# Performance work log

Hardware: AMD Instinct MI355X
Metric: run time of the kernel (lower is better)

## Reference

```python
import jax, jax.numpy as jnp
import numpy as np

NUM_HEADS = 32
HEAD_DIM = 64
ROPE_THETA = 10000.0


def _rope_cos_sin(position_ids, head_dim, theta):
    # inv_freq: [head_dim/2]
    half = head_dim // 2
    inv_freq = 1.0 / (theta ** (jnp.arange(0, half, dtype=jnp.float32) * 2.0 / head_dim))
    angles = position_ids.astype(jnp.float32)[..., None] * inv_freq  # [B,S,half]
    return jnp.cos(angles), jnp.sin(angles)


def _apply_rope(x, cos, sin):
    # x: [B,S,H,hd]; cos/sin: [B,S,half] -> broadcast over heads (rotate-half, Llama style)
    half = x.shape[-1] // 2
    x1, x2 = x[..., :half], x[..., half:]
    c = cos[:, :, None, :]
    s = sin[:, :, None, :]
    return jnp.concatenate([x1 * c - x2 * s, x2 * c + x1 * s], axis=-1)


def setup_inputs() -> dict:
    key = jax.random.key(0)
    ks = jax.random.split(key, 8)
    B, S, D = 2, 2048, 2048
    hidden_states = jax.random.normal(ks[0], (B, S, D), dtype=jnp.float32)
    # causal additive mask (is_causal=False in IpexSDP; mask carries causality)
    causal = jnp.tril(jnp.ones((S, S), dtype=jnp.bool_))
    attention_mask = jnp.where(causal, 0.0, -1e9).astype(jnp.float32)[None, None, :, :]
    attention_mask = jnp.broadcast_to(attention_mask, (B, 1, S, S))
    position_ids = jnp.broadcast_to(jnp.arange(S, dtype=jnp.int64)[None, :], (B, S))
    scale = 0.02
    qkv_w = jax.random.normal(ks[1], (3, D, D), dtype=jnp.float32) * scale
    qkv_b = jax.random.normal(ks[2], (3, D), dtype=jnp.float32) * scale
    o_w = jax.random.normal(ks[3], (D, D), dtype=jnp.float32) * scale
    o_b = jax.random.normal(ks[4], (D,), dtype=jnp.float32) * scale
    residual = jax.random.normal(ks[5], (B, S, D), dtype=jnp.float32)
    return {
        'hidden_states': hidden_states,
        'attention_mask': attention_mask,
        'position_ids': position_ids,
        'qkv_w': qkv_w,
        'qkv_b': qkv_b,
        'o_w': o_w,
        'o_b': o_b,
        'residual': residual,
    }


def reference(hidden_states, attention_mask, position_ids, qkv_w, qkv_b, o_w, o_b, residual):
    B, S, D = hidden_states.shape
    H, hd = NUM_HEADS, HEAD_DIM
    # fused QKV projection (weights stored transposed: x @ W), matching mm_qkv_out
    qkv = jnp.einsum('bsd,tde->tbse', hidden_states, qkv_w) + qkv_b[:, None, None, :]
    q = qkv[0].reshape(B, S, H, hd)
    k = qkv[1].reshape(B, S, H, hd)
    v = qkv[2].reshape(B, S, H, hd)
    cos, sin = _rope_cos_sin(position_ids, hd, ROPE_THETA)
    q = _apply_rope(q, cos, sin)
    k = _apply_rope(k, cos, sin)
    scale = 1.0 / jnp.sqrt(jnp.asarray(hd, dtype=hidden_states.dtype))
    # [B,H,S,S]
    scores = jnp.einsum('bqhd,bkhd->bhqk', q, k) * scale + attention_mask
    probs = jax.nn.softmax(scores, axis=-1)
    attn = jnp.einsum('bhqk,bkhd->bqhd', probs, v).reshape(B, S, D)
    # o-proj fused with bias + residual add (matmul_add_add)
    out = attn @ o_w + o_b + residual
    return out
```

## Files before the change

### kernel.cpp

```cpp
#include <hip/hip_runtime.h>
#include <stdint.h>
#include <stdio.h>

#define D_MODEL 2048
#define SEQ     2048
#define NHEADS  32
#define HDIM    64
#define BATCH   2
#define BH      (BATCH * NHEADS)
#define GK      2048

typedef unsigned short u16;
typedef unsigned int   u32;
typedef __attribute__((ext_vector_type(8))) short short8;
typedef __attribute__((ext_vector_type(4))) short s16x4;
typedef __attribute__((ext_vector_type(4))) float f32x4;
typedef __attribute__((ext_vector_type(4))) u32   u32x4;
typedef __attribute__((ext_vector_type(2))) u32   u32x2;

__device__ __forceinline__ float bf2f(u16 x) {
  union { u32 u; float f; } c; c.u = ((u32)x) << 16; return c.f;
}
__device__ __forceinline__ u16 f2bf(float f) {
  union { float f; u32 u; } c; c.f = f;
  u32 u = c.u;
  return (u16)((u + 0x7FFFu + ((u >> 16) & 1u)) >> 16);
}
__device__ __forceinline__ u32 fbits(float f) {
  union { float f; u32 u; } c; c.f = f; return c.u;
}

typedef const __attribute__((address_space(1))) u32* gas_t;
typedef __attribute__((address_space(3))) u32* las_t;
__device__ __forceinline__ void gll16(const void* g, void* l) {
  __builtin_amdgcn_global_load_lds((gas_t)g, (las_t)l, 16, 0, 0);
}
__device__ __forceinline__ u32 lds_addr(const void* p) {
  return (u32)(size_t)(const __attribute__((address_space(3))) void*)p;
}
__device__ __forceinline__ short8 ds_read128(u32 addr) {
  short8 r;
  asm volatile("ds_read_b128 %0, %1" : "=v"(r) : "v"(addr));
  return r;
}

__device__ __forceinline__ void swiz_mn(int pid, int nx, int& mtile, int& ntile) {
  int chunk = 8 * nx;
  int grp = pid / chunk, loc = pid - grp * chunk;
  mtile = grp * 8 + (loc & 7);
  ntile = loc >> 3;
}

__global__ __launch_bounds__(256) void cvt_k(const float* __restrict__ in,
                                             u16* __restrict__ out) {
  int id = blockIdx.x * 256 + threadIdx.x;
  f32x4 v = *(const f32x4*)&in[(size_t)id * 4];
  alignas(8) u16 o[4];
#pragma unroll
  for (int j = 0; j < 4; j++) o[j] = f2bf(v[j]);
  *(u32x2*)&out[(size_t)id * 4] = *(const u32x2*)o;
}

__global__ __launch_bounds__(256) void transpose_cvt_k(const float* __restrict__ qkv_w,
                                                       const float* __restrict__ o_w,
                                                       u16* __restrict__ outT) {
  __shared__ u16 tile[64][72];
  const int z = blockIdx.z;
  const float* inz = (z < 3) ? qkv_w + (size_t)z * D_MODEL * D_MODEL : o_w;
  u16* outz = outT + (size_t)z * D_MODEL * D_MODEL;
  const int r0 = blockIdx.y * 64, c0 = blockIdx.x * 64;
  const int t = threadIdx.x;
  const int lrow = t >> 4, lcol4 = (t & 15) * 4;
#pragma unroll
  for (int i = 0; i < 4; i++) {
    int r = lrow + i * 16;
    f32x4 v = *(const f32x4*)&inz[(size_t)(r0 + r) * D_MODEL + (c0 + lcol4)];
#pragma unroll
    for (int j = 0; j < 4; j++) tile[r][lcol4 + j] = f2bf(v[j]);
  }
  __syncthreads();
  const int row = t >> 3, col8 = (t & 7) * 8;
#pragma unroll
  for (int i = 0; i < 2; i++) {
    int r = row + i * 32;
    alignas(16) u16 vals[8];
#pragma unroll
    for (int j = 0; j < 8; j++) vals[j] = tile[col8 + j][r];
    *(u32x4*)&outz[(size_t)(c0 + r) * D_MODEL + (r0 + col8)] = *(const u32x4*)vals;
  }
}

__device__ __forceinline__ void gemm128(const u16* __restrict__ A, const u16* __restrict__ BT,
                                        int m0, int n0, u16* As, u16* Bs, f32x4 acc[4][4]) {
  const int t = threadIdx.x;
  const int lane = t & 63, w = t >> 6;
  const int quad = lane >> 4, l16 = lane & 15;
  const int wr = w >> 1, wc = w & 1;
  const int ldr = lane >> 2, ldc = (lane & 3) * 8;
#pragma unroll
  for (int mt = 0; mt < 4; mt++)
#pragma unroll
    for (int nt = 0; nt < 4; nt++)
#pragma unroll
      for (int i = 0; i < 4; i++) acc[mt][nt][i] = 0.0f;

  for (int k0 = 0; k0 < GK; k0 += 32) {
    __syncthreads();
#pragma unroll
    for (int i = 0; i < 2; i++) {
      int rbase = w * 32 + i * 16;
      gll16(&A[(size_t)(m0 + rbase + ldr) * GK + k0 + ldc], &As[rbase * 32]);
      gll16(&BT[(size_t)(n0 + rbase + ldr) * GK + k0 + ldc], &Bs[rbase * 32]);
    }
    __syncthreads();
    short8 af[4], bf[4];
#pragma unroll
    for (int mt = 0; mt < 4; mt++)
      af[mt] = *(const short8*)&As[(wr * 64 + mt * 16 + l16) * 32 + quad * 8];
#pragma unroll
    for (int nt = 0; nt < 4; nt++)
      bf[nt] = *(const short8*)&Bs[(wc * 64 + nt * 16 + l16) * 32 + quad * 8];
#pragma unroll
    for (int mt = 0; mt < 4; mt++)
#pragma unroll
      for (int nt = 0; nt < 4; nt++)
        acc[mt][nt] = __builtin_amdgcn_mfma_f32_16x16x32_bf16(af[mt], bf[nt], acc[mt][nt], 0, 0, 0);
  }
}


__device__ __forceinline__ void stage_half(const u16* __restrict__ src, int rowbase, int k0,
                                           u16* tile, int h, int w, int srl, int scol) {
  u16* ldsb = tile + h * (128 * 64);
  const u16* g0 = &src[(size_t)(rowbase + h * 128 + srl) * GK + k0 + scol];
  const u16* g1 = &src[(size_t)(rowbase + h * 128 + srl + 8) * GK + k0 + scol];
  gll16(g0, (char*)ldsb + w * 2048);
  gll16(g1, (char*)ldsb + w * 2048 + 1024);
}

#define LGKM0_FENCE  do { asm volatile("s_waitcnt lgkmcnt(0)"); __builtin_amdgcn_sched_barrier(0); } while (0)

__global__ __launch_bounds__(512, 1) void qkv_gemm256_k(const u16* __restrict__ A,
                                                        const u16* __restrict__ BT,
                                                        const float* __restrict__ bias,
                                                        u16* __restrict__ Qb, u16* __restrict__ Kb,
                                                        u16* __restrict__ Vbt) {
  __shared__ u16 As[2][256 * 64];
  __shared__ u16 Bs[2][256 * 64];
  const int t = threadIdx.x, w = t >> 6, lane = t & 63;
  const int quad = lane >> 4, l16 = lane & 15;
  const int wr = w >> 2, wc = w & 3;
  int mtile, ntile;
  swiz_mn(blockIdx.x, 24, mtile, ntile);
  const int m0 = mtile * 256, n0 = ntile * 256;
  const int srl = w * 16 + (lane >> 3);
  const int scol = (((lane & 7) ^ (lane >> 3)) << 3);

  const u32 asb0 = lds_addr(As[0]), asb1 = lds_addr(As[1]);
  const u32 bsb0 = lds_addr(Bs[0]), bsb1 = lds_addr(Bs[1]);
  const u32 xorc = (u32)((l16 & 7) << 4);
  const u32 cq0 = (u32)(quad * 16) ^ xorc;
  const u32 cq1 = (u32)(64 + quad * 16) ^ xorc;

  f32x4 acc[8][4];
#pragma unroll
  for (int mf = 0; mf < 8; mf++)
#pragma unroll
    for (int nf = 0; nf < 4; nf++)
#pragma unroll
      for (int i = 0; i < 4; i++) acc[mf][nf][i] = 0.0f;

  const int NT = GK / 64;
  stage_half(A, m0, 0, As[0], 0, w, srl, scol);
  stage_half(A, m0, 0, As[0], 1, w, srl, scol);
  stage_half(BT, n0, 0, Bs[0], 0, w, srl, scol);
  stage_half(BT, n0, 0, Bs[0], 1, w, srl, scol);
  stage_half(A, m0, 64, As[1], 0, w, srl, scol);
  stage_half(A, m0, 64, As[1], 1, w, srl, scol);
  asm volatile("s_waitcnt vmcnt(4)");
  __builtin_amdgcn_sched_barrier(0);
  __builtin_amdgcn_s_barrier();

  for (int kt = 0; kt < NT; kt++) {
    const int cur = kt & 1;
    const u32 aA = cur ? asb1 : asb0;
    const u32 aB = cur ? bsb1 : bsb0;
    u16* Acur = cur ? (u16*)As[1] : (u16*)As[0];
    u16* Bnxt = cur ? (u16*)Bs[0] : (u16*)Bs[1];
    short8 af[8][2], bf[4][2];
#pragma unroll
    for (int mf = 0; mf < 4; mf++) {
      u32 rb = aA + (u32)((wr * 128 + mf * 16 + l16) * 128);
      af[mf][0] = ds_read128(rb + cq0);
      af[mf][1] = ds_read128(rb + cq1);
    }
#pragma unroll
    for (int nf = 0; nf < 2; nf++) {
      u32 rb = aB + (u32)((wc * 64 + nf * 16 + l16) * 128);
      bf[nf][0] = ds_read128(rb + cq0);
      bf[nf][1] = ds_read128(rb + cq1);
    }
    if (kt + 1 < NT) stage_half(BT, n0, (kt + 1) * 64, Bnxt, 0, w, srl, scol);
    __builtin_amdgcn_s_barrier();
    LGKM0_FENCE;
    __builtin_amdgcn_s_setprio(1);
#pragma unroll
    for (int mf = 0; mf < 4; mf++)
#pragma unroll
      for (int nf = 0; nf < 2; nf++) {
        acc[mf][nf] = __builtin_amdgcn_mfma_f32_16x16x32_bf16(af[mf][0], bf[nf][0], acc[mf][nf], 0, 0, 0);
        acc[mf][nf] = __builtin_amdgcn_mfma_f32_16x16x32_bf16(af[mf][1], bf[nf][1], acc[mf][nf], 0, 0, 0);
      }
    __builtin_amdgcn_s_setprio(0);
    __builtin_amdgcn_s_barrier();
    __builtin_amdgcn_sched_barrier(0);
#pragma unroll
    for (int mf = 4; mf < 8; mf++) {
      u32 rb = aA + (u32)((wr * 128 + mf * 16 + l16) * 128);
      af[mf][0] = ds_read128(rb + cq0);
      af[mf][1] = ds_read128(rb + cq1);
    }
    if (kt + 1 < NT) stage_half(BT, n0, (kt + 1) * 64, Bnxt, 1, w, srl, scol);
    __builtin_amdgcn_s_barrier();
    LGKM0_FENCE;
    __builtin_amdgcn_s_setprio(1);
#pragma unroll
    for (int mf = 4; mf < 8; mf++)
#pragma unroll
      for (int nf = 0; nf < 2; nf++) {
        acc[mf][nf] = __builtin_amdgcn_mfma_f32_16x16x32_bf16(af[mf][0], bf[nf][0], acc[mf][nf], 0, 0, 0);
        acc[mf][nf] = __builtin_amdgcn_mfma_f32_16x16x32_bf16(af[mf][1], bf[nf][1], acc[mf][nf], 0, 0, 0);
      }
    __builtin_amdgcn_s_setprio(0);
    __builtin_amdgcn_s_barrier();
    __builtin_amdgcn_sched_barrier(0);
#pragma unroll
    for (int nf = 2; nf < 4; nf++) {
      u32 rb = aB + (u32)((wc * 64 + nf * 16 + l16) * 128);
      bf[nf][0] = ds_read128(rb + cq0);
      bf[nf][1] = ds_read128(rb + cq1);
    }
    if (kt + 2 < NT) stage_half(A, m0, (kt + 2) * 64, Acur, 0, w, srl, scol);
    __builtin_amdgcn_s_barrier();
    LGKM0_FENCE;
    __builtin_amdgcn_s_setprio(1);
#pragma unroll
    for (int mf = 0; mf < 4; mf++)
#pragma unroll
      for (int nf = 2; nf < 4; nf++) {
        acc[mf][nf] = __builtin_amdgcn_mfma_f32_16x16x32_bf16(af[mf][0], bf[nf][0], acc[mf][nf], 0, 0, 0);
        acc[mf][nf] = __builtin_amdgcn_mfma_f32_16x16x32_bf16(af[mf][1], bf[nf][1], acc[mf][nf], 0, 0, 0);
      }
    __builtin_amdgcn_s_setprio(0);
    __builtin_amdgcn_s_barrier();
    __builtin_amdgcn_sched_barrier(0);
    if (kt + 2 < NT) stage_half(A, m0, (kt + 2) * 64, Acur, 1, w, srl, scol);
    __builtin_amdgcn_s_barrier();
    __builtin_amdgcn_s_setprio(1);
#pragma unroll
    for (int mf = 4; mf < 8; mf++)
#pragma unroll
      for (int nf = 2; nf < 4; nf++) {
        acc[mf][nf] = __builtin_amdgcn_mfma_f32_16x16x32_bf16(af[mf][0], bf[nf][0], acc[mf][nf], 0, 0, 0);
        acc[mf][nf] = __builtin_amdgcn_mfma_f32_16x16x32_bf16(af[mf][1], bf[nf][1], acc[mf][nf], 0, 0, 0);
      }
    __builtin_amdgcn_s_setprio(0);
    if (kt + 2 < NT) {
      asm volatile("s_waitcnt vmcnt(4)");
    } else {
      asm volatile("s_waitcnt vmcnt(0)");
    }
    __builtin_amdgcn_sched_barrier(0);
    __builtin_amdgcn_s_barrier();
    __builtin_amdgcn_sched_barrier(0);
  }

  const int tsel = n0 >> 11;
  if (tsel < 2) {
    u16* dst = tsel ? Kb : Qb;
#pragma unroll
    for (int p = 0; p < 2; p++) {
      int nlo = n0 + wc * 64 + p * 16 + l16;
      float blo = bias[nlo], bhi = bias[nlo + 32];
      int j = p * 16 + l16;
      float inv = __expf((float)j * -0.28782313662425572f);
      int h = (nlo & 2047) >> 6;
#pragma unroll
      for (int mf = 0; mf < 8; mf++) {
#pragma unroll
        for (int r = 0; r < 4; r++) {
          int m = m0 + wr * 128 + mf * 16 + quad * 4 + r;
          int b = m >> 11, s = m & (SEQ - 1);
          float sn, cs;
          __sincosf((float)s * inv, &sn, &cs);
          float x1 = acc[mf][p][r] + blo;
          float x2 = acc[mf][p + 2][r] + bhi;
          size_t base = ((size_t)((b * NHEADS + h) * SEQ + s)) * HDIM;
          dst[base + j]      = f2bf(x1 * cs - x2 * sn);
          dst[base + j + 32] = f2bf(x2 * cs + x1 * sn);
        }
      }
    }
  } else {
#pragma unroll
    for (int nf = 0; nf < 4; nf++) {
      int n = n0 + wc * 64 + nf * 16 + l16;
      float bv = bias[n];
      int e = n & 2047, h = e >> 6, d = e & 63;
#pragma unroll
      for (int mf = 0; mf < 8; mf++) {
        int m0r = m0 + wr * 128 + mf * 16 + quad * 4;
        int b = m0r >> 11, s0 = m0r & (SEQ - 1);
        alignas(8) u16 o4[4];
#pragma unroll
        for (int r = 0; r < 4; r++) o4[r] = f2bf(acc[mf][nf][r] + bv);
        *(u32x2*)&Vbt[((size_t)((b * NHEADS + h) * HDIM + d)) * SEQ + s0] = *(const u32x2*)o4;
      }
    }
  }
}

__global__ __launch_bounds__(256) void oproj_gemm_k(const u16* __restrict__ A, const u16* __restrict__ BT,
                                                    const float* __restrict__ bias,
                                                    const float* __restrict__ resid,
                                                    float* __restrict__ out) {
  __shared__ u16 As[128 * 32], Bs[128 * 32];
  f32x4 acc[4][4];
  int mtile, ntile;
  swiz_mn(blockIdx.x, 16, mtile, ntile);
  const int m0 = mtile * 128, n0 = ntile * 128;
  gemm128(A, BT, m0, n0, As, Bs, acc);
  const int t = threadIdx.x, lane = t & 63, quad = lane >> 4, l16 = lane & 15;
  const int w = t >> 6, wr = w >> 1, wc = w & 1;
#pragma unroll
  for (int nt = 0; nt < 4; nt++) {
    int n = n0 + wc * 64 + nt * 16 + l16;
    float bv = bias[n];
#pragma unroll
    for (int mt = 0; mt < 4; mt++) {
#pragma unroll
      for (int r = 0; r < 4; r++) {
        int m = m0 + wr * 64 + mt * 16 + quad * 4 + r;
        size_t oi = (size_t)m * D_MODEL + n;
        out[oi] = acc[mt][nt][r] + bv + resid[oi];
      }
    }
  }
}

__global__ __launch_bounds__(256, 2) void attn_k(const u16* __restrict__ Qb,
                                                 const u16* __restrict__ Kb,
                                                 const u16* __restrict__ Vbt,
                                                 u16* __restrict__ attn) {
  __shared__ u16 smem[128 * 72];
  u16* Ks = smem;
  u16* Vt = smem + 64 * 72;
  const int blk = blockIdx.x;
  const int bh = blk & 63, pi = blk >> 6;
  const int b = bh >> 5, h = bh & 31;
  const int t = threadIdx.x, w = t >> 6, lane = t & 63, quad = lane >> 4, l16 = lane & 15;
  const int qbT[2] = { pi * 128, (15 - pi) * 128 };
  const int qwT[2] = { qbT[0] + w * 32, qbT[1] + w * 32 };
  const size_t bho = (size_t)bh * SEQ * HDIM;
  const size_t vbo = (size_t)bh * HDIM * SEQ;
  const int kend = qbT[1] + 128;

  short8 qf[2][2][2];
#pragma unroll
  for (int Ti = 0; Ti < 2; Ti++)
#pragma unroll
    for (int qt = 0; qt < 2; qt++)
#pragma unroll
      for (int kd = 0; kd < 2; kd++) {
        short8 v = *(const short8*)&Qb[bho + (size_t)(qwT[Ti] + qt * 16 + l16) * HDIM + kd * 32 + quad * 8];
#pragma unroll
        for (int i = 0; i < 8; i++) {
          float f = bf2f((u16)v[i]) * 0.125f;
          v[i] = (short)f2bf(f);
        }
        qf[Ti][qt][kd] = v;
      }

  f32x4 Oacc[2][4][2];
  float mrow[2][2] = {{-1e30f, -1e30f}, {-1e30f, -1e30f}};
  float lrow[2][2] = {{0.0f, 0.0f}, {0.0f, 0.0f}};
#pragma unroll
  for (int Ti = 0; Ti < 2; Ti++)
#pragma unroll
    for (int dt = 0; dt < 4; dt++)
#pragma unroll
      for (int qt = 0; qt < 2; qt++)
#pragma unroll
        for (int i = 0; i < 4; i++) Oacc[Ti][dt][qt][i] = 0.0f;

  const int srow = t >> 3, sc8 = (t & 7) * 8;
  u32x4 kreg[2], vreg[2];

#pragma unroll
  for (int j = 0; j < 2; j++) {
    kreg[j] = *(const u32x4*)&Kb[bho + (size_t)(srow + j * 32) * HDIM + sc8];
    vreg[j] = *(const u32x4*)&Vbt[vbo + (size_t)(srow + j * 32) * SEQ + sc8];
  }
#pragma unroll
  for (int j = 0; j < 2; j++) {
    *(u32x4*)&Ks[(srow + j * 32) * 72 + sc8] = kreg[j];
    *(u32x4*)&Vt[(srow + j * 32) * 72 + sc8] = vreg[j];
  }
  __syncthreads();

  for (int key0 = 0; key0 < kend; key0 += 64) {
    const int nxt = key0 + 64;
    if (nxt < kend) {
#pragma unroll
      for (int j = 0; j < 2; j++) {
        kreg[j] = *(const u32x4*)&Kb[bho + (size_t)(nxt + srow + j * 32) * HDIM + sc8];
        vreg[j] = *(const u32x4*)&Vbt[vbo + (size_t)(srow + j * 32) * SEQ + nxt + sc8];
      }
    }
#pragma unroll
    for (int Ti = 0; Ti < 2; Ti++) {
      const int qw = qwT[Ti];
      if (key0 <= qw + 31) {
        const int lim = qw + 31 - key0;
        int nkt = (lim >> 4) + 1; if (nkt > 4) nkt = 4;
        f32x4 sacc[4][2];
#pragma unroll
        for (int kt = 0; kt < 4; kt++) {
          if (kt < nkt) {
            short8 kf0 = *(const short8*)&Ks[(kt * 16 + l16) * 72 + quad * 8];
            short8 kf1 = *(const short8*)&Ks[(kt * 16 + l16) * 72 + 32 + quad * 8];
#pragma unroll
            for (int qt = 0; qt < 2; qt++) {
              f32x4 z = {0.0f, 0.0f, 0.0f, 0.0f};
              z = __builtin_amdgcn_mfma_f32_16x16x32_bf16(kf0, qf[Ti][qt][0], z, 0, 0, 0);
              z = __builtin_amdgcn_mfma_f32_16x16x32_bf16(kf1, qf[Ti][qt][1], z, 0, 0, 0);
              sacc[kt][qt] = z;
            }
          }
        }
        if (key0 + 63 > qw) {
#pragma unroll
          for (int qt = 0; qt < 2; qt++) {
            int qrow = qw + qt * 16 + l16;
#pragma unroll
            for (int kt = 0; kt < 4; kt++)
              if (kt < nkt)
#pragma unroll
                for (int r = 0; r < 4; r++)
                  if (key0 + kt * 16 + quad * 4 + r > qrow) sacc[kt][qt][r] = -1e30f;
          }
        }
        float alpha[2];
#pragma unroll
        for (int qt = 0; qt < 2; qt++) {
          float mx = -1e30f;
#pragma unroll
          for (int kt = 0; kt < 4; kt++)
            if (kt < nkt)
#pragma unroll
              for (int r = 0; r < 4; r++) mx = fmaxf(mx, sacc[kt][qt][r]);
          mx = fmaxf(mx, __shfl_xor(mx, 16));
          mx = fmaxf(mx, __shfl_xor(mx, 32));
          float mnew = fmaxf(mrow[Ti][qt], mx);
          alpha[qt] = __expf(mrow[Ti][qt] - mnew);
          mrow[Ti][qt] = mnew;
          float rsum = 0.0f;
#pragma unroll
          for (int kt = 0; kt < 4; kt++)
            if (kt < nkt)
#pragma unroll
              for (int r = 0; r < 4; r++) {
                float pv = __expf(sacc[kt][qt][r] - mnew);
                sacc[kt][qt][r] = pv;
                rsum += pv;
              }
          rsum += __shfl_xor(rsum, 16);
          rsum += __shfl_xor(rsum, 32);
          lrow[Ti][qt] = lrow[Ti][qt] * alpha[qt] + rsum;
        }
#pragma unroll
        for (int dt = 0; dt < 4; dt++)
#pragma unroll
          for (int qt = 0; qt < 2; qt++)
#pragma unroll
            for (int r = 0; r < 4; r++) Oacc[Ti][dt][qt][r] *= alpha[qt];
#pragma unroll
        for (int kt = 0; kt < 4; kt++) {
          if (kt < nkt) {
            s16x4 pk[2];
#pragma unroll
            for (int qt = 0; qt < 2; qt++) {
              u32 a0 = fbits(sacc[kt][qt][0]) + 0x8000u;
              u32 a1 = fbits(sacc[kt][qt][1]) + 0x8000u;
              u32 a2 = fbits(sacc[kt][qt][2]) + 0x8000u;
              u32 a3 = fbits(sacc[kt][qt][3]) + 0x8000u;
              union { u32 u[2]; s16x4 s; } pc;
              pc.u[0] = __builtin_amdgcn_perm(a1, a0, 0x07060302u);
              pc.u[1] = __builtin_amdgcn_perm(a3, a2, 0x07060302u);
              pk[qt] = pc.s;
            }
            s16x4 vf[4];
#pragma unroll
            for (int dt = 0; dt < 4; dt++)
              vf[dt] = *(const s16x4*)&Vt[(dt * 16 + l16) * 72 + kt * 16 + quad * 4];
#pragma unroll
            for (int dt = 0; dt < 4; dt++)
#pragma unroll
              for (int qt = 0; qt < 2; qt++)
                Oacc[Ti][dt][qt] = __builtin_amdgcn_mfma_f32_16x16x16bf16_1k(vf[dt], pk[qt], Oacc[Ti][dt][qt], 0, 0, 0);
          }
        }
      }
    }
    __syncthreads();
    if (nxt < kend) {
#pragma unroll
      for (int j = 0; j < 2; j++) {
        *(u32x4*)&Ks[(srow + j * 32) * 72 + sc8] = kreg[j];
        *(u32x4*)&Vt[(srow + j * 32) * 72 + sc8] = vreg[j];
      }
      __syncthreads();
    }
  }

#pragma unroll
  for (int Ti = 0; Ti < 2; Ti++) {
    float invl[2] = {1.0f / lrow[Ti][0], 1.0f / lrow[Ti][1]};
#pragma unroll
    for (int dt = 0; dt < 4; dt++)
#pragma unroll
      for (int qt = 0; qt < 2; qt++)
#pragma unroll
        for (int r = 0; r < 4; r++)
          smem[(w * 32 + qt * 16 + l16) * 72 + dt * 16 + quad * 4 + r] =
              f2bf(Oacc[Ti][dt][qt][r] * invl[qt]);
    __syncthreads();
#pragma unroll
    for (int ii = 0; ii < 4; ii++) {
      int chunk = t + ii * 256;
      int row = chunk >> 3, g = chunk & 7;
      *(u32x4*)&attn[((size_t)(b * SEQ + qbT[Ti] + row)) * D_MODEL + h * 64 + g * 8] =
          *(const u32x4*)&smem[row * 72 + g * 8];
    }
    __syncthreads();
  }
}

extern "C" void kernel_launch(void* const* d_in, const int* in_sizes, int n_in,
                              void* d_out, int out_size, void* d_ws, size_t ws_size,
                              hipStream_t stream) {
  (void)in_sizes; (void)n_in; (void)out_size;
  const float* hidden = (const float*)d_in[0];
  const float* qkv_w = (const float*)d_in[3];
  const float* qkv_b = (const float*)d_in[4];
  const float* o_w   = (const float*)d_in[5];
  const float* o_b   = (const float*)d_in[6];
  const float* resid = (const float*)d_in[7];
  float* out = (float*)d_out;

  u16* ws = (u16*)d_ws;
  size_t off = 0;
  u16* hidb  = ws + off; off += (size_t)BATCH * SEQ * D_MODEL;
  u16* qkvT  = ws + off; off += (size_t)3 * D_MODEL * D_MODEL;
  u16* owT   = ws + off; off += (size_t)D_MODEL * D_MODEL;
  u16* Qb    = ws + off; off += (size_t)BH * SEQ * HDIM;
  u16* Kb    = ws + off; off += (size_t)BH * SEQ * HDIM;
  u16* Vbt   = ws + off; off += (size_t)BH * SEQ * HDIM;
  u16* attnb = ws + off; off += (size_t)BATCH * SEQ * D_MODEL;
  if (ws_size < off * sizeof(u16)) {
    fprintf(stderr, "kernel_launch: workspace too small: need %zu bytes, have %zu\n",
            off * sizeof(u16), ws_size);
    return;
  }
  (void)owT;

  cvt_k<<<(BATCH * SEQ * D_MODEL) / (4 * 256), 256, 0, stream>>>(hidden, hidb);
  transpose_cvt_k<<<dim3(32, 32, 4), 256, 0, stream>>>(qkv_w, o_w, qkvT);
  qkv_gemm256_k<<<16 * 24, 512, 0, stream>>>(hidb, qkvT, qkv_b, Qb, Kb, Vbt);
  attn_k<<<BH * 8, 256, 0, stream>>>(Qb, Kb, Vbt, attnb);
  oproj_gemm_k<<<16 * 32, 256, 0, stream>>>(attnb, owT, o_b, resid, out);
}
```

Baseline: 426.1 us.

## Restructure QKV GEMM K-loop: issue all LDS reads upfront with immediate offsets, fewer barriers

The QKV GEMM main loop now issues all A and B fragment LDS reads for a k-step at the start, using ds_read_b128 with immediate offsets from precomputed base addresses. It then waits on partial lgkmcnt counts so MFMA groups can start while later reads are still in flight. The B-tile global-to-LDS stages are merged into one point and the A-tile stages into another, which drops several workgroup barriers per iteration. This cuts address arithmetic and synchronisation stalls. The cost is more live fragment registers and a hand-counted lgkmcnt sequence that must stay consistent with the interleaved global_load_lds traffic.

```diff
diff --git a/kernel.cpp b/kernel.cpp
--- a/kernel.cpp
+++ b/kernel.cpp
@@ -38,9 +38,10 @@
 __device__ __forceinline__ u32 lds_addr(const void* p) {
   return (u32)(size_t)(const __attribute__((address_space(3))) void*)p;
 }
-__device__ __forceinline__ short8 ds_read128(u32 addr) {
+template <int OFF>
+__device__ __forceinline__ short8 ds_read128o(u32 addr) {
   short8 r;
-  asm volatile("ds_read_b128 %0, %1" : "=v"(r) : "v"(addr));
+  asm volatile("ds_read_b128 %0, %1 offset:%2" : "=v"(r) : "v"(addr), "i"(OFF));
   return r;
 }
 
@@ -138,7 +139,7 @@
   gll16(g1, (char*)ldsb + w * 2048 + 1024);
 }
 
-#define LGKM0_FENCE  do { asm volatile("s_waitcnt lgkmcnt(0)"); __builtin_amdgcn_sched_barrier(0); } while (0)
+#define SBAR0 __builtin_amdgcn_sched_barrier(0)
 
 __global__ __launch_bounds__(512, 1) void qkv_gemm256_k(const u16* __restrict__ A,
                                                         const u16* __restrict__ BT,
@@ -161,6 +162,8 @@
   const u32 xorc = (u32)((l16 & 7) << 4);
   const u32 cq0 = (u32)(quad * 16) ^ xorc;
   const u32 cq1 = (u32)(64 + quad * 16) ^ xorc;
+  const u32 rowA = (u32)((wr * 128 + l16) * 128);
+  const u32 rowB = (u32)((wc * 64 + l16) * 128);
 
   f32x4 acc[8][4];
 #pragma unroll
@@ -178,31 +181,33 @@
   stage_half(A, m0, 64, As[1], 0, w, srl, scol);
   stage_half(A, m0, 64, As[1], 1, w, srl, scol);
   asm volatile("s_waitcnt vmcnt(4)");
-  __builtin_amdgcn_sched_barrier(0);
+  SBAR0;
   __builtin_amdgcn_s_barrier();
+
+#define RD_A(mf, kh) af[mf][kh] = ds_read128o<(mf) * 2048>((kh) ? bA1 : bA0)
+#define RD_B(nf, kh) bf[nf][kh] = ds_read128o<(nf) * 2048>((kh) ? bB1 : bB0)
 
   for (int kt = 0; kt < NT; kt++) {
     const int cur = kt & 1;
-    const u32 aA = cur ? asb1 : asb0;
-    const u32 aB = cur ? bsb1 : bsb0;
+    const u32 aAb = cur ? asb1 : asb0;
+    const u32 aBb = cur ? bsb1 : bsb0;
+    const u32 bA0 = aAb + rowA + cq0, bA1 = aAb + rowA + cq1;
+    const u32 bB0 = aBb + rowB + cq0, bB1 = aBb + rowB + cq1;
     u16* Acur = cur ? (u16*)As[1] : (u16*)As[0];
     u16* Bnxt = cur ? (u16*)Bs[0] : (u16*)Bs[1];
     short8 af[8][2], bf[4][2];
-#pragma unroll
-    for (int mf = 0; mf < 4; mf++) {
-      u32 rb = aA + (u32)((wr * 128 + mf * 16 + l16) * 128);
-      af[mf][0] = ds_read128(rb + cq0);
-      af[mf][1] = ds_read128(rb + cq1);
-    }
-#pragma unroll
-    for (int nf = 0; nf < 2; nf++) {
-      u32 rb = aB + (u32)((wc * 64 + nf * 16 + l16) * 128);
-      bf[nf][0] = ds_read128(rb + cq0);
-      bf[nf][1] = ds_read128(rb + cq1);
-    }
-    if (kt + 1 < NT) stage_half(BT, n0, (kt + 1) * 64, Bnxt, 0, w, srl, scol);
-    __builtin_amdgcn_s_barrier();
-    LGKM0_FENCE;
+    RD_A(0, 0); RD_A(0, 1); RD_A(1, 0); RD_A(1, 1);
+    RD_A(2, 0); RD_A(2, 1); RD_A(3, 0); RD_A(3, 1);
+    RD_B(0, 0); RD_B(0, 1); RD_B(1, 0); RD_B(1, 1);
+    RD_A(4, 0); RD_A(4, 1); RD_A(5, 0); RD_A(5, 1);
+    RD_A(6, 0); RD_A(6, 1); RD_A(7, 0); RD_A(7, 1);
+    RD_B(2, 0); RD_B(2, 1); RD_B(3, 0); RD_B(3, 1);
+    if (kt + 1 < NT) {
+      stage_half(BT, n0, (kt + 1) * 64, Bnxt, 0, w, srl, scol);
+      stage_half(BT, n0, (kt + 1) * 64, Bnxt, 1, w, srl, scol);
+    }
+    asm volatile("s_waitcnt lgkmcnt(12)");
+    SBAR0;
     __builtin_amdgcn_s_setprio(1);
 #pragma unroll
     for (int mf = 0; mf < 4; mf++)
@@ -212,17 +217,8 @@
         acc[mf][nf] = __builtin_amdgcn_mfma_f32_16x16x32_bf16(af[mf][1], bf[nf][1], acc[mf][nf], 0, 0, 0);
       }
     __builtin_amdgcn_s_setprio(0);
-    __builtin_amdgcn_s_barrier();
-    __builtin_amdgcn_sched_barrier(0);
-#pragma unroll
-    for (int mf = 4; mf < 8; mf++) {
-      u32 rb = aA + (u32)((wr * 128 + mf * 16 + l16) * 128);
-      af[mf][0] = ds_read128(rb + cq0);
-      af[mf][1] = ds_read128(rb + cq1);
-    }
-    if (kt + 1 < NT) stage_half(BT, n0, (kt + 1) * 64, Bnxt, 1, w, srl, scol);
-    __builtin_amdgcn_s_barrier();
-    LGKM0_FENCE;
+    asm volatile("s_waitcnt lgkmcnt(4)");
+    SBAR0;
     __builtin_amdgcn_s_setprio(1);
 #pragma unroll
     for (int mf = 4; mf < 8; mf++)
@@ -233,32 +229,16 @@
       }
     __builtin_amdgcn_s_setprio(0);
     __builtin_amdgcn_s_barrier();
-    __builtin_amdgcn_sched_barrier(0);
-#pragma unroll
-    for (int nf = 2; nf < 4; nf++) {
-      u32 rb = aB + (u32)((wc * 64 + nf * 16 + l16) * 128);
-      bf[nf][0] = ds_read128(rb + cq0);
-      bf[nf][1] = ds_read128(rb + cq1);
-    }
-    if (kt + 2 < NT) stage_half(A, m0, (kt + 2) * 64, Acur, 0, w, srl, scol);
-    __builtin_amdgcn_s_barrier();
-    LGKM0_FENCE;
+    SBAR0;
+    if (kt + 2 < NT) {
+      stage_half(A, m0, (kt + 2) * 64, Acur, 0, w, srl, scol);
+      stage_half(A, m0, (kt + 2) * 64, Acur, 1, w, srl, scol);
+    }
+    asm volatile("s_waitcnt lgkmcnt(0)");
+    SBAR0;
     __builtin_amdgcn_s_setprio(1);
 #pragma unroll
-    for (int mf = 0; mf < 4; mf++)
-#pragma unroll
-      for (int nf = 2; nf < 4; nf++) {
-        acc[mf][nf] = __builtin_amdgcn_mfma_f32_16x16x32_bf16(af[mf][0], bf[nf][0], acc[mf][nf], 0, 0, 0);
-        acc[mf][nf] = __builtin_amdgcn_mfma_f32_16x16x32_bf16(af[mf][1], bf[nf][1], acc[mf][nf], 0, 0, 0);
-      }
-    __builtin_amdgcn_s_setprio(0);
-    __builtin_amdgcn_s_barrier();
-    __builtin_amdgcn_sched_barrier(0);
-    if (kt + 2 < NT) stage_half(A, m0, (kt + 2) * 64, Acur, 1, w, srl, scol);
-    __builtin_amdgcn_s_barrier();
-    __builtin_amdgcn_s_setprio(1);
-#pragma unroll
-    for (int mf = 4; mf < 8; mf++)
+    for (int mf = 0; mf < 8; mf++)
 #pragma unroll
       for (int nf = 2; nf < 4; nf++) {
         acc[mf][nf] = __builtin_amdgcn_mfma_f32_16x16x32_bf16(af[mf][0], bf[nf][0], acc[mf][nf], 0, 0, 0);
@@ -270,10 +250,12 @@
     } else {
       asm volatile("s_waitcnt vmcnt(0)");
     }
-    __builtin_amdgcn_sched_barrier(0);
+    SBAR0;
     __builtin_amdgcn_s_barrier();
-    __builtin_amdgcn_sched_barrier(0);
-  }
+    SBAR0;
+  }
+#undef RD_A
+#undef RD_B
 
   const int tsel = n0 >> 11;
   if (tsel < 2) {
```

After: 417.1 us. 1.02x faster.
